# Performance work log

Hardware: AMD Instinct MI355X
Metric: run time of the kernel (lower is better)

The kernel has to match this reference:

```python
import jax, jax.numpy as jnp
import numpy as np

M = 512; N = 512; H = 1.0; DX = 1.0; DY = 1.0
NUM_ITERS = 600            # enough Jacobi iterations for the wavefront to cross a 512x512 grid
Q = 4000000                # num_event * num_station query points
INF = 1e5                  # 'infinity' initialization for travel times


def eikonal_solve(f_flat, m1, n1):
    """Parallel (Jacobi) fast-iterative Eikonal solve |grad u| = f on an MxN grid,
    Godunov upwind update, source at (m1, n1). Converges to the same viscosity
    solution as the original C++ fast-sweeping kernel."""
    f = f_flat.reshape(M, N)
    fh = f * H
    u0 = jnp.full((M, N), INF, dtype=f_flat.dtype).at[m1, n1].set(0.0)

    def step(u, _):
        up = jnp.pad(u, 1, constant_values=INF)
        a = jnp.minimum(up[:-2, 1:-1], up[2:, 1:-1])   # min over x-neighbors
        b = jnp.minimum(up[1:-1, :-2], up[1:-1, 2:])   # min over y-neighbors
        one_sided = jnp.minimum(a, b) + fh
        disc = 2.0 * fh * fh - (a - b) ** 2
        two_sided = 0.5 * (a + b + jnp.sqrt(jnp.maximum(disc, 0.0)))
        u_new = jnp.where(jnp.abs(a - b) >= fh, one_sided, two_sided)
        u = jnp.minimum(u, u_new).at[m1, n1].set(0.0)
        return u, None

    u, _ = jax.lax.scan(step, u0, None, length=NUM_ITERS)
    return u.reshape(-1)


def bilinear(u, gridx, gridy):
    """Faithful translation of the module's gather-based bilinear interpolation,
    including the original's quirks (f_x2y1 used for both w12 and w21 terms,
    f_x1y2 computed but unused)."""
    xu = jnp.ceil(gridx); xl = jnp.floor(gridx)
    yu = jnp.ceil(gridy); yl = jnp.floor(gridy)
    g_uu = (xu * N + yu).astype(jnp.int32)
    g_ul = (xu * N + yl).astype(jnp.int32)
    g_lu = (xl * N + yu).astype(jnp.int32)
    g_ll = (xl * N + yl).astype(jnp.int32)
    f_x2y2 = u[g_uu]
    f_x2y1 = u[g_ul]
    f_x1y1 = u[g_ll]
    f_x1y2 = u[g_lu]  # computed but unused, as in the source
    xh = xu - gridx; xlw = gridx - xl
    yh = yu - gridy; ylw = gridy - yl
    w11 = xh * yh; w12 = xh * ylw; w21 = xlw * yh; w22 = xlw * ylw
    return (w11 * f_x1y1 + w12 * f_x2y1 + w21 * f_x2y1 + w22 * f_x2y2) * (1.0 / (DX * DY))


def setup_inputs() -> dict:
    key = jax.random.key(0)
    kf, kx, ky = jax.random.split(key, 3)
    f = 0.5 + jax.random.uniform(kf, (M * N,), jnp.float32)           # slowness field ~U[0.5,1.5]
    gridx = jax.random.uniform(kx, (Q,), jnp.float32) * (M - 2)       # query x in [0, M-2]
    gridy = jax.random.uniform(ky, (Q,), jnp.float32) * (N - 2)       # query y in [0, N-2]
    return {"f": f, "gridx": gridx, "gridy": gridy, "m1": 256, "n1": 256}


def reference(f, gridx, gridy, m1, n1):
    u = eikonal_solve(f, m1, n1)
    return bilinear(u, gridx, gridy)
```

## Files before the change

### kernel.cpp

```cpp
#include <hip/hip_runtime.h>

#define M_    512
#define N_    512
#define INF_  1e5f
#define FBIG  1e30f
#define T_    32
#define K_    24
#define TW    80
#define SD    88
#define QPR   20
#define NQ    (78*QPR)
#define NT    1024

#if !__has_builtin(__builtin_amdgcn_sqrtf)
#define __builtin_amdgcn_sqrtf sqrtf
#endif

__global__ __launch_bounds__(256) void init_u(float* __restrict__ u,
                                              const int* __restrict__ m1p,
                                              const int* __restrict__ n1p) {
    int idx = blockIdx.x * 256 + threadIdx.x;
    int src = m1p[0] * N_ + n1p[0];
    if (idx < M_ * N_) u[idx] = (idx == src) ? 0.0f : INF_;
}

__device__ __forceinline__ float cell_upd(float xn0, float xn1, float yn0, float yn1,
                                          float uc, float fh, float t2) {
    float a   = fminf(xn0, xn1);
    float b   = fminf(yn0, yn1);
    float amb = a - b;
    float one = fminf(a, b) + fh;
    float dis = fmaf(-amb, amb, t2);
    float two = 0.5f * (a + b + __builtin_amdgcn_sqrtf(fmaxf(dis, 0.0f)));
    float un  = (fabsf(amb) >= fh) ? one : two;
    return fminf(uc, un);
}

__device__ __forceinline__ void quad_update(const float* __restrict__ cur,
                                            float* __restrict__ nxt, int off4,
                                            const float* __restrict__ fq,
                                            const float* __restrict__ tq) {
    const int off = off4 * 4;
    float4 up = *(const float4*)(cur + off - SD);
    float4 dn = *(const float4*)(cur + off + SD);
    float4 ct = *(const float4*)(cur + off);
    float  lf = cur[off - 1];
    float  rt = cur[off + 4];
    float4 o;
    o.x = cell_upd(up.x, dn.x, lf,   ct.y, ct.x, fq[0], tq[0]);
    o.y = cell_upd(up.y, dn.y, ct.x, ct.z, ct.y, fq[1], tq[1]);
    o.z = cell_upd(up.z, dn.z, ct.y, ct.w, ct.z, fq[2], tq[2]);
    o.w = cell_upd(up.w, dn.w, ct.z, rt,   ct.w, fq[3], tq[3]);
    *(float4*)(nxt + off) = o;
}

__global__ __launch_bounds__(NT) void jacobi_k(const float* __restrict__ u_in,
                                               float* __restrict__ u_out,
                                               const float* __restrict__ f) {
    __shared__ float sA[TW * SD];
    __shared__ float sB[TW * SD];
    const int tid = threadIdx.x;
    const int bx  = blockIdx.x & 15;
    const int by  = blockIdx.x >> 4;
    const int gr0 = by * T_ - K_;
    const int gc0 = bx * T_ - K_;

    for (int idx = tid; idx < TW * TW; idx += NT) {
        int r = idx / TW, c = idx - r * TW;
        int gr = gr0 + r, gc = gc0 + c;
        float uv = INF_;
        if ((unsigned)gr < (unsigned)M_ && (unsigned)gc < (unsigned)N_)
            uv = u_in[gr * N_ + gc];
        sA[r * SD + c + 3] = uv;
    }

    int off0, off1 = 0, life0, life1 = 0;
    float fq0[4], tq0[4], fq1[4], tq1[4];
    {
        int qr = tid / QPR, qk = tid - qr * QPR;
        int r0 = qr + 1, c0 = 1 + 4 * qk;
        off0  = 22 * r0 + 1 + qk;
        life0 = min(min(r0, 79 - r0), min(c0 + 3, 79 - c0));
        #pragma unroll
        for (int j = 0; j < 4; ++j) {
            int gr = gr0 + r0, gc = gc0 + c0 + j;
            float fv = FBIG;
            if ((unsigned)gr < (unsigned)M_ && (unsigned)gc < (unsigned)N_)
                fv = f[gr * N_ + gc];
            fq0[j] = fv; tq0[j] = 2.0f * fv * fv;
        }
    }
    if (tid + NT < NQ) {
        int qi = tid + NT;
        int qr = qi / QPR, qk = qi - qr * QPR;
        int r1 = qr + 1, c1 = 1 + 4 * qk;
        off1  = 22 * r1 + 1 + qk;
        life1 = min(min(r1, 79 - r1), min(c1 + 3, 79 - c1));
        #pragma unroll
        for (int j = 0; j < 4; ++j) {
            int gr = gr0 + r1, gc = gc0 + c1 + j;
            float fv = FBIG;
            if ((unsigned)gr < (unsigned)M_ && (unsigned)gc < (unsigned)N_)
                fv = f[gr * N_ + gc];
            fq1[j] = fv; tq1[j] = 2.0f * fv * fv;
        }
    }
    __syncthreads();

    float* cur = sA;
    float* nxt = sB;
    for (int t = 0; t < K_; ++t) {
        if (t < life0) quad_update(cur, nxt, off0, fq0, tq0);
        if (t < life1) quad_update(cur, nxt, off1, fq1, tq1);
        __syncthreads();
        float* tmp = cur; cur = nxt; nxt = tmp;
    }

    {
        int r = tid >> 5, c = tid & 31;
        u_out[(by * T_ + r) * N_ + bx * T_ + c] = cur[(K_ + r) * SD + (K_ + 3 + c)];
    }
}

__device__ __forceinline__ float bil1(const float* __restrict__ u, float gx, float gy) {
    float xu = ceilf(gx),  xl = floorf(gx);
    float yu = ceilf(gy),  yl = floorf(gy);
    int guu = (int)(xu * (float)N_ + yu);
    int gul = (int)(xu * (float)N_ + yl);
    int gll = (int)(xl * (float)N_ + yl);
    float f22 = u[guu];
    float f21 = u[gul];
    float f11 = u[gll];
    float xh = xu - gx, xlw = gx - xl;
    float yh = yu - gy, ylw = gy - yl;
    float w11 = xh * yh, w12 = xh * ylw, w21 = xlw * yh, w22 = xlw * ylw;
    return w11 * f11 + w12 * f21 + w21 * f21 + w22 * f22;
}

__global__ __launch_bounds__(256) void bilin(const float* __restrict__ u,
                                             const float* __restrict__ gx,
                                             const float* __restrict__ gy,
                                             float* __restrict__ out, int q4) {
    int i = blockIdx.x * blockDim.x + threadIdx.x;
    int stride = gridDim.x * blockDim.x;
    for (; i < q4; i += stride) {
        float4 x = reinterpret_cast<const float4*>(gx)[i];
        float4 y = reinterpret_cast<const float4*>(gy)[i];
        float4 o;
        o.x = bil1(u, x.x, y.x);
        o.y = bil1(u, x.y, y.y);
        o.z = bil1(u, x.z, y.z);
        o.w = bil1(u, x.w, y.w);
        reinterpret_cast<float4*>(out)[i] = o;
    }
}

extern "C" void kernel_launch(void* const* d_in, const int* in_sizes, int n_in,
                              void* d_out, int out_size, void* d_ws, size_t ws_size,
                              hipStream_t stream) {
    const float* f  = (const float*)d_in[0];
    const float* gx = (const float*)d_in[1];
    const float* gy = (const float*)d_in[2];
    const int*   m1 = (const int*)d_in[3];
    const int*   n1 = (const int*)d_in[4];
    float* out = (float*)d_out;

    float* ua = (float*)d_ws;
    float* ub = ua + M_ * N_;
    const int Q = in_sizes[1];

    init_u<<<(M_ * N_ + 255) / 256, 256, 0, stream>>>(ua, m1, n1);

    const float* src = ua;
    float*       dst = ub;
    for (int l = 0; l < 25; ++l) {
        jacobi_k<<<256, NT, 0, stream>>>(src, dst, f);
        float* t = (float*)src; src = dst; dst = t;
    }

    bilin<<<4096, 256, 0, stream>>>(src, gx, gy, out, Q / 4);
}
```

Before: 724.6 us.

## Halve Jacobi tile height to launch 512 blocks and fold init into first pass

```diff
diff --git a/kernel.cpp b/kernel.cpp
--- a/kernel.cpp
+++ b/kernel.cpp
@@ -4,25 +4,19 @@
 #define N_    512
 #define INF_  1e5f
 #define FBIG  1e30f
-#define T_    32
+#define TR    16
+#define TC    32
 #define K_    24
-#define TW    80
+#define TWR   64
+#define TWC   80
 #define SD    88
 #define QPR   20
-#define NQ    (78*QPR)
+#define NQ    (62*QPR)
 #define NT    1024
 
 #if !__has_builtin(__builtin_amdgcn_sqrtf)
 #define __builtin_amdgcn_sqrtf sqrtf
 #endif
-
-__global__ __launch_bounds__(256) void init_u(float* __restrict__ u,
-                                              const int* __restrict__ m1p,
-                                              const int* __restrict__ n1p) {
-    int idx = blockIdx.x * 256 + threadIdx.x;
-    int src = m1p[0] * N_ + n1p[0];
-    if (idx < M_ * N_) u[idx] = (idx == src) ? 0.0f : INF_;
-}
 
 __device__ __forceinline__ float cell_upd(float xn0, float xn1, float yn0, float yn1,
                                           float uc, float fh, float t2) {
@@ -56,21 +50,28 @@
 
 __global__ __launch_bounds__(NT) void jacobi_k(const float* __restrict__ u_in,
                                                float* __restrict__ u_out,
-                                               const float* __restrict__ f) {
-    __shared__ float sA[TW * SD];
-    __shared__ float sB[TW * SD];
+                                               const float* __restrict__ f,
+                                               const int* __restrict__ m1p,
+                                               const int* __restrict__ n1p,
+                                               int first) {
+    __shared__ float sA[TWR * SD];
+    __shared__ float sB[TWR * SD];
     const int tid = threadIdx.x;
     const int bx  = blockIdx.x & 15;
     const int by  = blockIdx.x >> 4;
-    const int gr0 = by * T_ - K_;
-    const int gc0 = bx * T_ - K_;
+    const int gr0 = by * TR - K_;
+    const int gc0 = bx * TC - K_;
+    const int srcR = m1p[0], srcC = n1p[0];
 
-    for (int idx = tid; idx < TW * TW; idx += NT) {
-        int r = idx / TW, c = idx - r * TW;
+    for (int idx = tid; idx < TWR * TWC; idx += NT) {
+        int r = idx / TWC, c = idx - r * TWC;
         int gr = gr0 + r, gc = gc0 + c;
         float uv = INF_;
-        if ((unsigned)gr < (unsigned)M_ && (unsigned)gc < (unsigned)N_)
-            uv = u_in[gr * N_ + gc];
+        if (first) {
+            uv = (gr == srcR && gc == srcC) ? 0.0f : INF_;
+        } else if ((unsigned)gr < (unsigned)M_ && (unsigned)gc < (unsigned)N_) {
+            uv = u_in[(gr << 9) + gc];
+        }
         sA[r * SD + c + 3] = uv;
     }
 
@@ -80,13 +81,13 @@
         int qr = tid / QPR, qk = tid - qr * QPR;
         int r0 = qr + 1, c0 = 1 + 4 * qk;
         off0  = 22 * r0 + 1 + qk;
-        life0 = min(min(r0, 79 - r0), min(c0 + 3, 79 - c0));
+        life0 = min(min(r0, 63 - r0), min(c0 + 3, 79 - c0));
         #pragma unroll
         for (int j = 0; j < 4; ++j) {
             int gr = gr0 + r0, gc = gc0 + c0 + j;
             float fv = FBIG;
             if ((unsigned)gr < (unsigned)M_ && (unsigned)gc < (unsigned)N_)
-                fv = f[gr * N_ + gc];
+                fv = f[(gr << 9) + gc];
             fq0[j] = fv; tq0[j] = 2.0f * fv * fv;
         }
     }
@@ -95,13 +96,13 @@
         int qr = qi / QPR, qk = qi - qr * QPR;
         int r1 = qr + 1, c1 = 1 + 4 * qk;
         off1  = 22 * r1 + 1 + qk;
-        life1 = min(min(r1, 79 - r1), min(c1 + 3, 79 - c1));
+        life1 = min(min(r1, 63 - r1), min(c1 + 3, 79 - c1));
         #pragma unroll
         for (int j = 0; j < 4; ++j) {
             int gr = gr0 + r1, gc = gc0 + c1 + j;
             float fv = FBIG;
             if ((unsigned)gr < (unsigned)M_ && (unsigned)gc < (unsigned)N_)
-                fv = f[gr * N_ + gc];
+                fv = f[(gr << 9) + gc];
             fq1[j] = fv; tq1[j] = 2.0f * fv * fv;
         }
     }
@@ -116,9 +117,9 @@
         float* tmp = cur; cur = nxt; nxt = tmp;
     }
 
-    {
+    if (tid < TR * TC) {
         int r = tid >> 5, c = tid & 31;
-        u_out[(by * T_ + r) * N_ + bx * T_ + c] = cur[(K_ + r) * SD + (K_ + 3 + c)];
+        u_out[((by * TR + r) << 9) + bx * TC + c] = cur[(K_ + r) * SD + (K_ + 3 + c)];
     }
 }
 
@@ -169,12 +170,10 @@
     float* ub = ua + M_ * N_;
     const int Q = in_sizes[1];
 
-    init_u<<<(M_ * N_ + 255) / 256, 256, 0, stream>>>(ua, m1, n1);
-
-    const float* src = ua;
-    float*       dst = ub;
+    const float* src = ub;
+    float*       dst = ua;
     for (int l = 0; l < 25; ++l) {
-        jacobi_k<<<256, NT, 0, stream>>>(src, dst, f);
+        jacobi_k<<<512, NT, 0, stream>>>(src, dst, f, m1, n1, l == 0 ? 1 : 0);
         float* t = (float*)src; src = dst; dst = t;
     }
 
```

Measured after the change: 867.2 us. +19.7%, slower.
